# Optimization experiments

Hardware: AMD Instinct MI355X
Metric: run time of the kernel (lower is better)

The kernel has to match this reference:

```python
import jax, jax.numpy as jnp
import numpy as np

B, NQ, D = 8, 900, 256
NH, NL, NP = 8, 4, 4
DFF = 1024
DH = D // NH
SHAPES = [(100, 100), (50, 50), (25, 25), (13, 13)]
LV = sum(h * w for h, w in SHAPES)


def setup_inputs() -> dict:
    key = jax.random.key(0)
    ks = iter(jax.random.split(key, 40))
    nrm = lambda shape, s=0.02: jax.random.normal(next(ks), shape, jnp.float32) * s
    starts = np.cumsum([0] + [h * w for h, w in SHAPES[:-1]])
    return {
        'query': jax.random.normal(next(ks), (B, NQ, D), jnp.float32),
        'reference_points': jax.random.uniform(next(ks), (B, NQ, NL, 2), jnp.float32),
        'memory': jax.random.normal(next(ks), (B, LV, D), jnp.float32),
        'memory_spatial_shapes': jnp.array(SHAPES, jnp.int32),
        'level_start_index': jnp.array(starts, jnp.int32),
        'memory_key_padding_mask': jnp.zeros((B, LV), bool),
        'in_proj_w': nrm((3 * D, D)), 'in_proj_b': jnp.zeros((3 * D,), jnp.float32),
        'out_proj_w': nrm((D, D)), 'out_proj_b': jnp.zeros((D,), jnp.float32),
        'ln1_g': jnp.ones((D,), jnp.float32), 'ln1_b': jnp.zeros((D,), jnp.float32),
        'value_proj_w': nrm((D, D)), 'value_proj_b': jnp.zeros((D,), jnp.float32),
        'samp_off_w': nrm((NH * NL * NP * 2, D)), 'samp_off_b': nrm((NH * NL * NP * 2,), 1.0),
        'attn_w_w': nrm((NH * NL * NP, D)), 'attn_w_b': jnp.zeros((NH * NL * NP,), jnp.float32),
        'ca_out_w': nrm((D, D)), 'ca_out_b': jnp.zeros((D,), jnp.float32),
        'ln2_g': jnp.ones((D,), jnp.float32), 'ln2_b': jnp.zeros((D,), jnp.float32),
        'ffn_w1': nrm((DFF, D)), 'ffn_b1': jnp.zeros((DFF,), jnp.float32),
        'ffn_w2': nrm((D, DFF)), 'ffn_b2': jnp.zeros((D,), jnp.float32),
        'ln3_g': jnp.ones((D,), jnp.float32), 'ln3_b': jnp.zeros((D,), jnp.float32),
    }


def layer_norm(x, g, b):
    m = x.mean(-1, keepdims=True)
    v = jnp.var(x, axis=-1, keepdims=True)
    return (x - m) * jax.lax.rsqrt(v + 1e-5) * g + b


def self_attention(x, in_w, in_b, out_w, out_b):
    qkv = x @ in_w.T + in_b
    q, k, v = jnp.split(qkv, 3, axis=-1)
    b, n, _ = x.shape
    q = q.reshape(b, n, NH, DH)
    k = k.reshape(b, n, NH, DH)
    v = v.reshape(b, n, NH, DH)
    scores = jnp.einsum('bqhd,bkhd->bhqk', q, k) / jnp.sqrt(jnp.float32(DH))
    attn = jax.nn.softmax(scores, axis=-1)
    o = jnp.einsum('bhqk,bkhd->bqhd', attn, v).reshape(b, n, D)
    return o @ out_w.T + out_b


def ms_deform_attn(value, shapes, loc, aw):
    # value: (B, Lv, NH, DH); loc: (B, Nq, NH, NL, NP, 2) in [0,1]; aw: (B, Nq, NH, NL, NP)
    b, _, nh, dh = value.shape
    nq, p = loc.shape[1], loc.shape[4]
    acc = jnp.zeros((b, nh, nq, dh), value.dtype)
    start = 0
    for lvl, (hl, wl) in enumerate(shapes):
        v = value[:, start:start + hl * wl].transpose(0, 2, 1, 3)  # (B, NH, HW, DH)
        start += hl * wl
        g = loc[:, :, :, lvl]                      # (B, Nq, NH, NP, 2)
        x = g[..., 0] * wl - 0.5
        y = g[..., 1] * hl - 0.5
        x0 = jnp.floor(x); y0 = jnp.floor(y)
        lx = x - x0; ly = y - y0

        def gather(yi, xi):
            valid = (yi >= 0) & (yi < hl) & (xi >= 0) & (xi < wl)
            idx = (jnp.clip(yi, 0, hl - 1) * wl + jnp.clip(xi, 0, wl - 1)).astype(jnp.int32)
            idx = idx.transpose(0, 2, 1, 3).reshape(b, nh, nq * p)
            out = jnp.take_along_axis(v, idx[..., None], axis=2)  # (B, NH, Nq*NP, DH)
            m = valid.transpose(0, 2, 1, 3).reshape(b, nh, nq * p, 1)
            return jnp.where(m, out, 0.0)

        def w_(w):  # (B,Nq,NH,NP) -> (B,NH,Nq*NP,1)
            return w.transpose(0, 2, 1, 3).reshape(b, nh, nq * p, 1)

        samp = (gather(y0, x0) * w_((1 - lx) * (1 - ly))
                + gather(y0, x0 + 1) * w_(lx * (1 - ly))
                + gather(y0 + 1, x0) * w_((1 - lx) * ly)
                + gather(y0 + 1, x0 + 1) * w_(lx * ly))
        samp = samp.reshape(b, nh, nq, p, dh)
        wl_attn = aw[:, :, :, lvl].transpose(0, 2, 1, 3)  # (B, NH, Nq, NP)
        acc = acc + jnp.einsum('bhqpd,bhqp->bhqd', samp, wl_attn)
    return acc.transpose(0, 2, 1, 3).reshape(b, nq, nh * dh)


def reference(query, reference_points, memory, memory_spatial_shapes, level_start_index,
              memory_key_padding_mask, in_proj_w, in_proj_b, out_proj_w, out_proj_b,
              ln1_g, ln1_b, value_proj_w, value_proj_b, samp_off_w, samp_off_b,
              attn_w_w, attn_w_b, ca_out_w, ca_out_b, ln2_g, ln2_b,
              ffn_w1, ffn_b1, ffn_w2, ffn_b2, ln3_g, ln3_b):
    shapes = [(int(h), int(w)) for h, w in np.asarray(memory_spatial_shapes)]
    b, nq, _ = query.shape

    # self-attention + LN residual
    q_sa = self_attention(query, in_proj_w, in_proj_b, out_proj_w, out_proj_b)
    query = layer_norm(query + q_sa, ln1_g, ln1_b)

    # deformable cross-attention
    value = memory @ value_proj_w.T + value_proj_b
    value = jnp.where(memory_key_padding_mask[..., None], 0.0, value)
    value = value.reshape(b, -1, NH, DH)
    offsets = (query @ samp_off_w.T + samp_off_b).reshape(b, nq, NH, NL, NP, 2)
    aw = (query @ attn_w_w.T + attn_w_b).reshape(b, nq, NH, NL * NP)
    aw = jax.nn.softmax(aw, axis=-1).reshape(b, nq, NH, NL, NP)
    normalizer = jnp.stack([memory_spatial_shapes[:, 1], memory_spatial_shapes[:, 0]], -1).astype(query.dtype)  # (NL,2)=(W,H)
    loc = reference_points[:, :, None, :, None, :] + offsets / normalizer[None, None, None, :, None, :]
    q_ca = ms_deform_attn(value, shapes, loc, aw) @ ca_out_w.T + ca_out_b
    query = layer_norm(query + q_ca, ln2_g, ln2_b)

    # FFN + LN residual
    q_ffn = jax.nn.relu(query @ ffn_w1.T + ffn_b1) @ ffn_w2.T + ffn_b2
    return layer_norm(query + q_ffn, ln3_g, ln3_b)
```

## Files before the change

### kernel.cpp

```cpp
#include <hip/hip_runtime.h>
#include <cstddef>

namespace {

constexpr int kB   = 8;
constexpr int kNQ  = 900;
constexpr int kD   = 256;
constexpr int kDFF = 1024;
constexpr int kLV  = 13294;

typedef short bf16x8 __attribute__((ext_vector_type(8)));
typedef float f32x4  __attribute__((ext_vector_type(4)));

__device__ inline unsigned short f2bf(float f) {
  union { float f; unsigned u; } v; v.f = f;
  return (unsigned short)((v.u + 0x7FFF + ((v.u >> 16) & 1)) >> 16);
}

__device__ inline float bf2f(unsigned short u) {
  union { unsigned u; float f; } v; v.u = (unsigned)u << 16;
  return v.f;
}

__device__ inline unsigned cvt_pk_bf16(float a, float b) {
  unsigned r;
  asm("v_cvt_pk_bf16_f32 %0, %1, %2" : "=v"(r) : "v"(a), "v"(b));
  return r;
}

__global__ __launch_bounds__(256) void f32_to_bf16_kernel(
    const float* __restrict__ in, unsigned* __restrict__ out, int n8) {
  int i = blockIdx.x * 256 + threadIdx.x;
  const int stride = gridDim.x * 256;
  for (; i < n8; i += stride) {
    const float4 a = ((const float4*)in)[(size_t)i * 2];
    const float4 b = ((const float4*)in)[(size_t)i * 2 + 1];
    uint4 r;
    r.x = cvt_pk_bf16(a.x, a.y);
    r.y = cvt_pk_bf16(a.z, a.w);
    r.z = cvt_pk_bf16(b.x, b.y);
    r.w = cvt_pk_bf16(b.z, b.w);
    ((uint4*)out)[i] = r;
  }
}

__global__ __launch_bounds__(256, 2) void gemm_val2_kernel(
    const unsigned short* __restrict__ A, const float* __restrict__ W,
    const float* __restrict__ bias, unsigned short* __restrict__ C, int M) {
  __shared__ short Ws[128 * 256];

  const int t  = threadIdx.x;
  const int w  = t >> 6;
  const int l  = t & 63;
  const int lr = l & 15;
  const int lc = l >> 4;
  const int col  = (int)(blockIdx.x >> 8);
  const int slot = (int)(blockIdx.x & 255);
  const int bn = col * 128;
  const int wm = (w >> 1) * 64;
  const int wn = (w & 1) * 64;

#pragma unroll 4
  for (int i = 0; i < 16; ++i) {
    const int idx = i * 256 + t;
    const int row = idx >> 5;
    const int c16 = idx & 31;
    const float* wp = W + (size_t)(bn + row) * 256 + c16 * 8;
    const float4 w0 = *(const float4*)wp;
    const float4 w1 = *(const float4*)(wp + 4);
    uint4 p;
    p.x = cvt_pk_bf16(w0.x, w0.y);
    p.y = cvt_pk_bf16(w0.z, w0.w);
    p.z = cvt_pk_bf16(w1.x, w1.y);
    p.w = cvt_pk_bf16(w1.z, w1.w);
    const int boff = (row * 512 + c16 * 16) ^ ((row & 7) << 4);
    *(uint4*)((char*)Ws + boff) = p;
  }
  __syncthreads();

  float bv[4];
#pragma unroll
  for (int n = 0; n < 4; ++n) bv[n] = bias[bn + wn + n * 16 + lr];

  for (int tile = slot; tile * 128 < M; tile += 256) {
    const int bm = tile * 128;

    const unsigned short* apm[4];
#pragma unroll
    for (int m = 0; m < 4; ++m) {
      int row = bm + wm + m * 16 + lr;
      row = row < M ? row : M - 1;
      apm[m] = A + (size_t)row * 256 + lc * 8;
    }
    bf16x8 af[8][4];
#pragma unroll
    for (int kk = 0; kk < 8; ++kk)
#pragma unroll
      for (int m = 0; m < 4; ++m)
        af[kk][m] = *(const bf16x8*)(apm[m] + kk * 32);

    f32x4 acc[4][4];
#pragma unroll
    for (int m = 0; m < 4; ++m)
#pragma unroll
      for (int n = 0; n < 4; ++n) acc[m][n] = (f32x4){0.f, 0.f, 0.f, 0.f};

#pragma unroll
    for (int kk = 0; kk < 8; ++kk) {
      const int kb = kk * 64 + lc * 16;
      bf16x8 bfr[4];
#pragma unroll
      for (int n = 0; n < 4; ++n) {
        const int row = wn + n * 16 + lr;
        const int boff = (row * 512 + kb) ^ ((row & 7) << 4);
        bfr[n] = *(const bf16x8*)((const char*)Ws + boff);
      }
#pragma unroll
      for (int m = 0; m < 4; ++m)
#pragma unroll
        for (int n = 0; n < 4; ++n)
          acc[m][n] = __builtin_amdgcn_mfma_f32_16x16x32_bf16(af[kk][m], bfr[n], acc[m][n], 0, 0, 0);
    }

#pragma unroll
    for (int m = 0; m < 4; ++m) {
      const int rbase = bm + wm + m * 16 + lc * 4;
#pragma unroll
      for (int n = 0; n < 4; ++n) {
        const int cidx = bn + wn + n * 16 + lr;
#pragma unroll
        for (int j = 0; j < 4; ++j) {
          const int r = rbase + j;
          if (r < M) C[(size_t)r * 256 + cidx] = f2bf(acc[m][n][j] + bv[n]);
        }
      }
    }
  }
}

__global__ __launch_bounds__(256) void gemm_mfma_kernel(
    const float* __restrict__ A, const float* __restrict__ W,
    const float* __restrict__ bias, void* __restrict__ Cv,
    int M, int N, int K, int relu, int out_bf16) {
  __shared__ short As[128 * 64];
  __shared__ short Bs[128 * 64];

  const int t  = threadIdx.x;
  const int bm = blockIdx.y * 128;
  const int bn = blockIdx.x * 128;
  const int w  = t >> 6;
  const int l  = t & 63;
  const int wm = (w >> 1) * 64;
  const int wn = (w & 1) * 64;

  f32x4 acc[4][4];
#pragma unroll
  for (int m = 0; m < 4; ++m)
#pragma unroll
    for (int n = 0; n < 4; ++n) acc[m][n] = (f32x4){0.f, 0.f, 0.f, 0.f};

  float4 pa[8], pw[8];
  auto load_tile = [&](int k0) {
#pragma unroll
    for (int i = 0; i < 8; ++i) {
      const int slot = i * 256 + t;
      const int row  = slot >> 4;
      const int c4   = slot & 15;
      const int ar   = bm + row;
      pa[i] = (ar < M) ? *(const float4*)(A + (size_t)ar * K + k0 + c4 * 4)
                       : make_float4(0.f, 0.f, 0.f, 0.f);
      pw[i] = *(const float4*)(W + (size_t)(bn + row) * K + k0 + c4 * 4);
    }
  };

  load_tile(0);

  for (int k0 = 0;;) {
#pragma unroll
    for (int i = 0; i < 8; ++i) {
      const int slot = i * 256 + t;
      const int row  = slot >> 4;
      const int c4   = slot & 15;
      const int boff = (row * 128 + c4 * 8) ^ ((row & 7) << 4);
      uint2 ap;
      ap.x = cvt_pk_bf16(pa[i].x, pa[i].y);
      ap.y = cvt_pk_bf16(pa[i].z, pa[i].w);
      *(uint2*)((char*)As + boff) = ap;
      uint2 wp;
      wp.x = cvt_pk_bf16(pw[i].x, pw[i].y);
      wp.y = cvt_pk_bf16(pw[i].z, pw[i].w);
      *(uint2*)((char*)Bs + boff) = wp;
    }
    __syncthreads();

    const int knext = k0 + 64;
    if (knext < K) load_tile(knext);

#pragma unroll
    for (int ks = 0; ks < 2; ++ks) {
      const int koff = (ks * 32 + (l >> 4) * 8) * 2;
      bf16x8 af[4], bfr[4];
#pragma unroll
      for (int m = 0; m < 4; ++m) {
        const int row = wm + m * 16 + (l & 15);
        af[m] = *(const bf16x8*)((const char*)As + ((row * 128 + koff) ^ ((row & 7) << 4)));
      }
#pragma unroll
      for (int n = 0; n < 4; ++n) {
        const int row = wn + n * 16 + (l & 15);
        bfr[n] = *(const bf16x8*)((const char*)Bs + ((row * 128 + koff) ^ ((row & 7) << 4)));
      }
#pragma unroll
      for (int m = 0; m < 4; ++m)
#pragma unroll
        for (int n = 0; n < 4; ++n)
          acc[m][n] = __builtin_amdgcn_mfma_f32_16x16x32_bf16(af[m], bfr[n], acc[m][n], 0, 0, 0);
    }

    k0 = knext;
    if (k0 >= K) break;
    __syncthreads();
  }

  const int lr4 = (l >> 4) * 4;
  const int lc  = l & 15;
#pragma unroll
  for (int m = 0; m < 4; ++m) {
    const int rbase = bm + wm + m * 16 + lr4;
#pragma unroll
    for (int n = 0; n < 4; ++n) {
      const int col = bn + wn + n * 16 + lc;
      const float bv = bias[col];
#pragma unroll
      for (int j = 0; j < 4; ++j) {
        const int r = rbase + j;
        if (r < M) {
          float v = acc[m][n][j] + bv;
          if (relu) v = fmaxf(v, 0.f);
          if (out_bf16)
            ((unsigned short*)Cv)[(size_t)r * N + col] = f2bf(v);
          else
            ((float*)Cv)[(size_t)r * N + col] = v;
        }
      }
    }
  }
}

__global__ __launch_bounds__(256) void gemm_qoff_kernel(
    const float* __restrict__ A, const float* __restrict__ soW,
    const float* __restrict__ soB, const float* __restrict__ awW,
    const float* __restrict__ awB, float* __restrict__ offs,
    float* __restrict__ awr, int M) {
  __shared__ short As[128 * 64];
  __shared__ short Bs[128 * 64];

  const int t  = threadIdx.x;
  const int bm = blockIdx.y * 128;
  const int bn = blockIdx.x * 128;
  const int w  = t >> 6;
  const int l  = t & 63;
  const int wm = (w >> 1) * 64;
  const int wn = (w & 1) * 64;

  f32x4 acc[4][4];
#pragma unroll
  for (int m = 0; m < 4; ++m)
#pragma unroll
    for (int n = 0; n < 4; ++n) acc[m][n] = (f32x4){0.f, 0.f, 0.f, 0.f};

  float4 pa[8], pw[8];
  auto load_tile = [&](int k0) {
#pragma unroll
    for (int i = 0; i < 8; ++i) {
      const int slot = i * 256 + t;
      const int row  = slot >> 4;
      const int c4   = slot & 15;
      const int ar   = bm + row;
      pa[i] = (ar < M) ? *(const float4*)(A + (size_t)ar * 256 + k0 + c4 * 4)
                       : make_float4(0.f, 0.f, 0.f, 0.f);
      const int gn = bn + row;
      const float* Wp = (gn < 256) ? (soW + (size_t)gn * 256)
                                   : (awW + (size_t)(gn - 256) * 256);
      pw[i] = *(const float4*)(Wp + k0 + c4 * 4);
    }
  };

  load_tile(0);

  for (int k0 = 0;;) {
#pragma unroll
    for (int i = 0; i < 8; ++i) {
      const int slot = i * 256 + t;
      const int row  = slot >> 4;
      const int c4   = slot & 15;
      const int boff = (row * 128 + c4 * 8) ^ ((row & 7) << 4);
      uint2 ap;
      ap.x = cvt_pk_bf16(pa[i].x, pa[i].y);
      ap.y = cvt_pk_bf16(pa[i].z, pa[i].w);
      *(uint2*)((char*)As + boff) = ap;
      uint2 wp;
      wp.x = cvt_pk_bf16(pw[i].x, pw[i].y);
      wp.y = cvt_pk_bf16(pw[i].z, pw[i].w);
      *(uint2*)((char*)Bs + boff) = wp;
    }
    __syncthreads();

    const int knext = k0 + 64;
    if (knext < 256) load_tile(knext);

#pragma unroll
    for (int ks = 0; ks < 2; ++ks) {
      const int koff = (ks * 32 + (l >> 4) * 8) * 2;
      bf16x8 af[4], bfr[4];
#pragma unroll
      for (int m = 0; m < 4; ++m) {
        const int row = wm + m * 16 + (l & 15);
        af[m] = *(const bf16x8*)((const char*)As + ((row * 128 + koff) ^ ((row & 7) << 4)));
      }
#pragma unroll
      for (int n = 0; n < 4; ++n) {
        const int row = wn + n * 16 + (l & 15);
        bfr[n] = *(const bf16x8*)((const char*)Bs + ((row * 128 + koff) ^ ((row & 7) << 4)));
      }
#pragma unroll
      for (int m = 0; m < 4; ++m)
#pragma unroll
        for (int n = 0; n < 4; ++n)
          acc[m][n] = __builtin_amdgcn_mfma_f32_16x16x32_bf16(af[m], bfr[n], acc[m][n], 0, 0, 0);
    }

    k0 = knext;
    if (k0 >= 256) break;
    __syncthreads();
  }

  const int lr4 = (l >> 4) * 4;
  const int lc  = l & 15;
#pragma unroll
  for (int m = 0; m < 4; ++m) {
    const int rbase = bm + wm + m * 16 + lr4;
#pragma unroll
    for (int n = 0; n < 4; ++n) {
      const int col = bn + wn + n * 16 + lc;
      const float bv = (col < 256) ? soB[col] : awB[col - 256];
#pragma unroll
      for (int j = 0; j < 4; ++j) {
        const int r = rbase + j;
        if (r < M) {
          const float v = acc[m][n][j] + bv;
          if (col < 256) offs[(size_t)r * 256 + col] = v;
          else           awr[(size_t)r * 128 + col - 256] = v;
        }
      }
    }
  }
}

__global__ __launch_bounds__(256) void self_attn_mfma_kernel(
    const unsigned short* __restrict__ qkv, float* __restrict__ out) {
  const int b = blockIdx.y >> 3;
  const int h = blockIdx.y & 7;
  const int t = threadIdx.x;
  const int w = t >> 6;
  const int l = t & 63;
  const int lr = l & 15;
  const int lc = l >> 4;

  __shared__ short Klds[64 * 40];
  __shared__ short Vt[32 * 68];
  __shared__ short Plds[4][2 * 16 * 68];

  const float scale = 0.17677669529663687f;
  const int qb0 = blockIdx.x * 128 + w * 16;

  bf16x8 qf[2] = {};
#pragma unroll
  for (int qt = 0; qt < 2; ++qt) {
    const int qr = qb0 + qt * 64 + lr;
    if (qr < kNQ)
      qf[qt] = *(const bf16x8*)(qkv + ((size_t)(b * kNQ + qr)) * 768 + h * 32 + lc * 8);
  }

  f32x4 o[2][2];
#pragma unroll
  for (int qt = 0; qt < 2; ++qt)
#pragma unroll
    for (int dh = 0; dh < 2; ++dh) o[qt][dh] = (f32x4){0.f, 0.f, 0.f, 0.f};
  const f32x4 zero4 = {0.f, 0.f, 0.f, 0.f};
  float lsum[2] = {0.f, 0.f};

  const int skey = t & 63, sc = t >> 6;
  bf16x8 kreg = {}, vreg = {};
  auto load_kv = [&](int tb) {
    const int kr = tb + skey;
    if (kr < kNQ) {
      const unsigned short* p = qkv + ((size_t)(b * kNQ + kr)) * 768 + h * 32 + sc * 8;
      kreg = *(const bf16x8*)(p + 256);
      vreg = *(const bf16x8*)(p + 512);
    } else {
      kreg = (bf16x8){}; vreg = (bf16x8){};
    }
  };

  load_kv(0);

  for (int tb = 0; tb < kNQ; tb += 64) {
    *(bf16x8*)&Klds[skey * 40 + sc * 8] = kreg;
#pragma unroll
    for (int i = 0; i < 8; ++i) Vt[(sc * 8 + i) * 68 + skey] = vreg[i];
    __syncthreads();

    if (tb + 64 < kNQ) load_kv(tb + 64);

    f32x4 s[2][4];
#pragma unroll
    for (int kt = 0; kt < 4; ++kt) {
      bf16x8 kf = *(const bf16x8*)&Klds[(kt * 16 + lr) * 40 + lc * 8];
      s[0][kt] = __builtin_amdgcn_mfma_f32_16x16x32_bf16(kf, qf[0], zero4, 0, 0, 0);
      s[1][kt] = __builtin_amdgcn_mfma_f32_16x16x32_bf16(kf, qf[1], zero4, 0, 0, 0);
    }

#pragma unroll
    for (int qt = 0; qt < 2; ++qt) {
      short* Pw = Plds[w] + qt * (16 * 68);
      float ls = 0.f;
#pragma unroll
      for (int kt = 0; kt < 4; ++kt) {
        float p[4];
#pragma unroll
        for (int j = 0; j < 4; ++j) {
          const int kg = tb + kt * 16 + lc * 4 + j;
          const float e = __expf(s[qt][kt][j] * scale);
          p[j] = (kg < kNQ) ? e : 0.f;
          ls += p[j];
        }
        uint2 pk;
        pk.x = cvt_pk_bf16(p[0], p[1]);
        pk.y = cvt_pk_bf16(p[2], p[3]);
        *(uint2*)&Pw[lr * 68 + kt * 16 + lc * 4] = pk;
      }
      lsum[qt] += ls;
    }

    bf16x8 v00 = *(const bf16x8*)&Vt[lr * 68 + lc * 8];
    bf16x8 v01 = *(const bf16x8*)&Vt[lr * 68 + 32 + lc * 8];
    bf16x8 v10 = *(const bf16x8*)&Vt[(16 + lr) * 68 + lc * 8];
    bf16x8 v11 = *(const bf16x8*)&Vt[(16 + lr) * 68 + 32 + lc * 8];
#pragma unroll
    for (int qt = 0; qt < 2; ++qt) {
      const short* Pw = Plds[w] + qt * (16 * 68);
      bf16x8 pa0 = *(const bf16x8*)&Pw[lr * 68 + lc * 8];
      bf16x8 pa1 = *(const bf16x8*)&Pw[lr * 68 + 32 + lc * 8];
      o[qt][0] = __builtin_amdgcn_mfma_f32_16x16x32_bf16(pa0, v00, o[qt][0], 0, 0, 0);
      o[qt][0] = __builtin_amdgcn_mfma_f32_16x16x32_bf16(pa1, v01, o[qt][0], 0, 0, 0);
      o[qt][1] = __builtin_amdgcn_mfma_f32_16x16x32_bf16(pa0, v10, o[qt][1], 0, 0, 0);
      o[qt][1] = __builtin_amdgcn_mfma_f32_16x16x32_bf16(pa1, v11, o[qt][1], 0, 0, 0);
    }
    __syncthreads();
  }

#pragma unroll
  for (int qt = 0; qt < 2; ++qt) {
    float lt = lsum[qt];
    lt += __shfl_xor(lt, 16);
    lt += __shfl_xor(lt, 32);
#pragma unroll
    for (int j = 0; j < 4; ++j) {
      const float lq = __shfl(lt, lc * 4 + j);
      const int q = qb0 + qt * 64 + lc * 4 + j;
      if (q < kNQ) {
        const float inv = 1.f / lq;
        float* op = out + ((size_t)(b * kNQ + q)) * 256 + h * 32;
        op[lr]      = o[qt][0][j] * inv;
        op[16 + lr] = o[qt][1][j] * inv;
      }
    }
  }
}

__global__ __launch_bounds__(256) void ln_res_kernel(
    const float* __restrict__ x, const float* __restrict__ res,
    const float* __restrict__ g, const float* __restrict__ bta,
    float* __restrict__ out) {
  const int row = blockIdx.x;
  const int t = threadIdx.x;
  const size_t idx = (size_t)row * 256 + t;
  const float v = x[idx] + res[idx];
  float s = v, s2 = v * v;
#pragma unroll
  for (int mask = 1; mask < 64; mask <<= 1) {
    s  += __shfl_xor(s, mask);
    s2 += __shfl_xor(s2, mask);
  }
  __shared__ float ws[4], ws2[4];
  if ((t & 63) == 0) { ws[t >> 6] = s; ws2[t >> 6] = s2; }
  __syncthreads();
  const float S  = ws[0] + ws[1] + ws[2] + ws[3];
  const float S2 = ws2[0] + ws2[1] + ws2[2] + ws2[3];
  const float mean = S * (1.f / 256.f);
  const float var  = S2 * (1.f / 256.f) - mean * mean;
  const float rstd = rsqrtf(var + 1e-5f);
  out[idx] = (v - mean) * rstd * g[t] + bta[t];
}

__global__ __launch_bounds__(256) void deform_kernel(
    const unsigned short* __restrict__ value,
    const float* __restrict__ offs,
    const float* __restrict__ awr,
    const float* __restrict__ refp,
    float* __restrict__ out) {
  const int bq = blockIdx.x;
  const int b = bq / kNQ;
  const int t = threadIdx.x;

  __shared__ int2  cpk[128][4];
  __shared__ float part[4][256];

  if (t < 128) {
    const float a = awr[(size_t)bq * 128 + t];
    float mx = a;
#pragma unroll
    for (int mask = 1; mask < 16; mask <<= 1) mx = fmaxf(mx, __shfl_xor(mx, mask));
    const float e = __expf(a - mx);
    float se = e;
#pragma unroll
    for (int mask = 1; mask < 16; mask <<= 1) se += __shfl_xor(se, mask);
    const float aw = e / se;

    const int h = t >> 4, lp = t & 15, lvl = lp >> 2;
    const int HL[4] = {100, 50, 25, 13};
    const int WL[4] = {100, 50, 25, 13};
    const int ST[4] = {0, 10000, 12500, 13125};
    const int Hl = HL[lvl], Wl = WL[lvl], st = ST[lvl];
    const float rx = refp[((size_t)bq * 4 + lvl) * 2 + 0];
    const float ry = refp[((size_t)bq * 4 + lvl) * 2 + 1];
    const float ox = offs[(size_t)bq * 256 + h * 32 + lp * 2 + 0];
    const float oy = offs[(size_t)bq * 256 + h * 32 + lp * 2 + 1];
    const float x = rx * (float)Wl + ox - 0.5f;
    const float y = ry * (float)Hl + oy - 0.5f;
    const float x0f = floorf(x), y0f = floorf(y);
    const int x0 = (int)x0f, y0 = (int)y0f;
    const float lx = x - x0f, ly = y - y0f;
    const float wts[4] = {(1.f - lx) * (1.f - ly), lx * (1.f - ly),
                          (1.f - lx) * ly,         lx * ly};
    const int ys[4] = {y0, y0, y0 + 1, y0 + 1};
    const int xs[4] = {x0, x0 + 1, x0, x0 + 1};
    const int pos = lp * 8 + h;
#pragma unroll
    for (int c = 0; c < 4; ++c) {
      const int yy = ys[c], xx = xs[c];
      const bool valid = (yy >= 0) && (yy < Hl) && (xx >= 0) && (xx < Wl);
      const int yc = min(max(yy, 0), Hl - 1);
      const int xc = min(max(xx, 0), Wl - 1);
      const float wf = valid ? wts[c] * aw : 0.f;
      cpk[pos][c] = make_int2(st + yc * Wl + xc, __float_as_int(wf));
    }
  }
  __syncthreads();

  const int w  = t >> 6;
  const int q4 = t & 63;
  const int h  = q4 >> 3;
  const int ch = q4 * 4;
  const unsigned short* vb = value + (size_t)b * kLV * 256 + ch;

  float a0 = 0.f, a1 = 0.f, a2 = 0.f, a3 = 0.f;
#pragma unroll
  for (int si = 0; si < 4; ++si) {
    const int s = w * 4 + si;
#pragma unroll
    for (int c = 0; c < 4; ++c) {
      const int2 p = cpk[s * 8 + h][c];
      const float wt = __int_as_float(p.y);
      const uint2 v = *(const uint2*)(vb + (size_t)p.x * 256);
      a0 = fmaf(wt, bf2f((unsigned short)(v.x & 0xffff)), a0);
      a1 = fmaf(wt, bf2f((unsigned short)(v.x >> 16)), a1);
      a2 = fmaf(wt, bf2f((unsigned short)(v.y & 0xffff)), a2);
      a3 = fmaf(wt, bf2f((unsigned short)(v.y >> 16)), a3);
    }
  }
  *(float4*)&part[w][ch] = make_float4(a0, a1, a2, a3);
  __syncthreads();

  out[(size_t)bq * 256 + t] = part[0][t] + part[1][t] + part[2][t] + part[3][t];
}

}

extern "C" void kernel_launch(void* const* d_in, const int* in_sizes, int n_in,
                              void* d_out, int out_size, void* d_ws, size_t ws_size,
                              hipStream_t stream) {
  const float* query  = (const float*)d_in[0];
  const float* refp   = (const float*)d_in[1];
  const float* memory = (const float*)d_in[2];
  const float* in_w  = (const float*)d_in[6];
  const float* in_b  = (const float*)d_in[7];
  const float* out_w = (const float*)d_in[8];
  const float* out_b = (const float*)d_in[9];
  const float* ln1g  = (const float*)d_in[10];
  const float* ln1b  = (const float*)d_in[11];
  const float* vp_w  = (const float*)d_in[12];
  const float* vp_b  = (const float*)d_in[13];
  const float* so_w  = (const float*)d_in[14];
  const float* so_b  = (const float*)d_in[15];
  const float* aw_w  = (const float*)d_in[16];
  const float* aw_b  = (const float*)d_in[17];
  const float* ca_w  = (const float*)d_in[18];
  const float* ca_b  = (const float*)d_in[19];
  const float* ln2g  = (const float*)d_in[20];
  const float* ln2b  = (const float*)d_in[21];
  const float* f1_w  = (const float*)d_in[22];
  const float* f1_b  = (const float*)d_in[23];
  const float* f2_w  = (const float*)d_in[24];
  const float* f2_b  = (const float*)d_in[25];
  const float* ln3g  = (const float*)d_in[26];
  const float* ln3b  = (const float*)d_in[27];
  float* out = (float*)d_out;

  const int MQ = kB * kNQ;
  const int MV = kB * kLV;

  float* ws = (float*)d_ws;
  size_t o = 0;
  float* qkvr = ws;
  float* ffh  = ws;  o += (size_t)MQ * kDFF;
  float* sa   = ws + o;  o += (size_t)MQ * kD;
  float* q1   = ws + o;  o += (size_t)MQ * kD;
  float* valr = ws + o;  o += (size_t)MV * kD;
  float* offs = ws + o;  o += (size_t)MQ * kD;
  float* awr  = ws + o;  o += (size_t)MQ * 128;
  float* dfo  = ws + o;  o += (size_t)MQ * kD;
  float* q2   = ws + o;  o += (size_t)MQ * kD;
  float* tmp  = ws + o;  o += (size_t)MQ * kD;
  (void)ws_size; (void)in_sizes; (void)n_in; (void)out_size;

  unsigned short* qkv_bf = (unsigned short*)qkvr;
  unsigned short* val_bf = (unsigned short*)valr;
  unsigned short* m_bf   = (unsigned short*)(valr + (size_t)MV * kD / 2);

  const dim3 blk(256);
  auto g128 = [](int M, int N) { return dim3((unsigned)((N + 127) / 128), (unsigned)((M + 127) / 128)); };

  f32_to_bf16_kernel<<<2048, blk, 0, stream>>>(memory, (unsigned*)m_bf, MV * kD / 8);
  gemm_mfma_kernel<<<g128(MQ, 768), blk, 0, stream>>>(query, in_w, in_b, qkv_bf, MQ, 768, kD, 0, 1);
  self_attn_mfma_kernel<<<dim3((kNQ + 127) / 128, kB * 8), blk, 0, stream>>>(qkv_bf, sa);
  gemm_mfma_kernel<<<g128(MQ, kD), blk, 0, stream>>>(sa, out_w, out_b, tmp, MQ, kD, kD, 0, 0);
  ln_res_kernel<<<MQ, blk, 0, stream>>>(query, tmp, ln1g, ln1b, q1);
  gemm_val2_kernel<<<512, blk, 0, stream>>>(m_bf, vp_w, vp_b, val_bf, MV);
  gemm_qoff_kernel<<<dim3(3, (MQ + 127) / 128), blk, 0, stream>>>(
      q1, so_w, so_b, aw_w, aw_b, offs, awr, MQ);
  deform_kernel<<<MQ, blk, 0, stream>>>(val_bf, offs, awr, refp, dfo);
  gemm_mfma_kernel<<<g128(MQ, kD), blk, 0, stream>>>(dfo, ca_w, ca_b, tmp, MQ, kD, kD, 0, 0);
  ln_res_kernel<<<MQ, blk, 0, stream>>>(q1, tmp, ln2g, ln2b, q2);
  gemm_mfma_kernel<<<g128(MQ, kDFF), blk, 0, stream>>>(q2, f1_w, f1_b, ffh, MQ, kDFF, kD, 1, 0);
  gemm_mfma_kernel<<<g128(MQ, kD), blk, 0, stream>>>(ffh, f2_w, f2_b, tmp, MQ, kD, kDFF, 0, 0);
  ln_res_kernel<<<MQ, blk, 0, stream>>>(q2, tmp, ln3g, ln3b, out);
}
```

Measured before the change: 288.3 us.

## Fuse output GEMMs with residual LayerNorm and store FFN hidden in bf16

Adds a gemm_ln_kernel that computes a full 256-wide output row tile (16 rows per block) and applies bias, residual add and LayerNorm in the epilogue. It replaces the three GEMM+ln_res_kernel pairs, removing the tmp buffer round trip and three launches. The FFN hidden activation is now written as bf16 and read directly, halving that traffic. The trade-off is that each 16-row block reconverts the whole fp32 weight tile to bf16, which adds redundant weight loads and conversion work, and the small M tile lowers MFMA reuse.

```diff
diff --git a/kernel.cpp b/kernel.cpp
--- a/kernel.cpp
+++ b/kernel.cpp
@@ -247,6 +247,124 @@
   }
 }
 
+__global__ __launch_bounds__(256) void gemm_ln_kernel(
+    const void* __restrict__ Av, const float* __restrict__ W,
+    const float* __restrict__ bias, const float* __restrict__ res,
+    const float* __restrict__ g, const float* __restrict__ beta,
+    float* __restrict__ C, int M, int K, int a_bf16) {
+  __shared__ short As[16 * 64];
+  __shared__ short Bs[256 * 64];
+  __shared__ float pS[4][16], pS2[4][16];
+
+  const int t  = threadIdx.x;
+  const int w  = t >> 6;
+  const int l  = t & 63;
+  const int lr = l & 15;
+  const int lc = l >> 4;
+  const int bm = blockIdx.x * 16;
+  const int wn = w * 64;
+
+  f32x4 acc[4];
+#pragma unroll
+  for (int n = 0; n < 4; ++n) acc[n] = (f32x4){0.f, 0.f, 0.f, 0.f};
+
+  for (int k0 = 0; k0 < K; k0 += 64) {
+    if (a_bf16) {
+      if (t < 128) {
+        const int row = t >> 3, c8 = t & 7;
+        const bf16x8 av = *(const bf16x8*)((const unsigned short*)Av +
+                                           (size_t)(bm + row) * K + k0 + c8 * 8);
+        const int boff = (row * 128 + c8 * 16) ^ ((row & 7) << 4);
+        *(bf16x8*)((char*)As + boff) = av;
+      }
+    } else {
+      const int row = t >> 4, c4 = t & 15;
+      const float4 av = *(const float4*)((const float*)Av +
+                                         (size_t)(bm + row) * K + k0 + c4 * 4);
+      uint2 p;
+      p.x = cvt_pk_bf16(av.x, av.y);
+      p.y = cvt_pk_bf16(av.z, av.w);
+      const int boff = (row * 128 + c4 * 8) ^ ((row & 7) << 4);
+      *(uint2*)((char*)As + boff) = p;
+    }
+#pragma unroll
+    for (int i = 0; i < 16; ++i) {
+      const int slot = i * 256 + t;
+      const int row = slot >> 4, c4 = slot & 15;
+      const float4 wv = *(const float4*)(W + (size_t)row * K + k0 + c4 * 4);
+      uint2 p;
+      p.x = cvt_pk_bf16(wv.x, wv.y);
+      p.y = cvt_pk_bf16(wv.z, wv.w);
+      const int boff = (row * 128 + c4 * 8) ^ ((row & 7) << 4);
+      *(uint2*)((char*)Bs + boff) = p;
+    }
+    __syncthreads();
+
+#pragma unroll
+    for (int ks = 0; ks < 2; ++ks) {
+      const int koff = (ks * 32 + lc * 8) * 2;
+      const bf16x8 af = *(const bf16x8*)((const char*)As + ((lr * 128 + koff) ^ ((lr & 7) << 4)));
+      bf16x8 bfr[4];
+#pragma unroll
+      for (int n = 0; n < 4; ++n) {
+        const int row = wn + n * 16 + lr;
+        bfr[n] = *(const bf16x8*)((const char*)Bs + ((row * 128 + koff) ^ ((row & 7) << 4)));
+      }
+#pragma unroll
+      for (int n = 0; n < 4; ++n)
+        acc[n] = __builtin_amdgcn_mfma_f32_16x16x32_bf16(af, bfr[n], acc[n], 0, 0, 0);
+    }
+    __syncthreads();
+  }
+
+  float bv[4], gl[4], bl[4];
+#pragma unroll
+  for (int n = 0; n < 4; ++n) {
+    const int col = wn + n * 16 + lr;
+    bv[n] = bias[col];
+    gl[n] = g[col];
+    bl[n] = beta[col];
+  }
+
+  float v[4][4];
+#pragma unroll
+  for (int j = 0; j < 4; ++j) {
+    const int grow = bm + lc * 4 + j;
+    float sj = 0.f, s2j = 0.f;
+#pragma unroll
+    for (int n = 0; n < 4; ++n) {
+      const int col = wn + n * 16 + lr;
+      const float vv = acc[n][j] + bv[n] + res[(size_t)grow * 256 + col];
+      v[j][n] = vv;
+      sj += vv;
+      s2j += vv * vv;
+    }
+#pragma unroll
+    for (int mask = 1; mask < 16; mask <<= 1) {
+      sj  += __shfl_xor(sj, mask);
+      s2j += __shfl_xor(s2j, mask);
+    }
+    if (lr == 0) { pS[w][lc * 4 + j] = sj; pS2[w][lc * 4 + j] = s2j; }
+  }
+  __syncthreads();
+
+#pragma unroll
+  for (int j = 0; j < 4; ++j) {
+    const int r16 = lc * 4 + j;
+    const float S  = pS[0][r16] + pS[1][r16] + pS[2][r16] + pS[3][r16];
+    const float S2 = pS2[0][r16] + pS2[1][r16] + pS2[2][r16] + pS2[3][r16];
+    const float mean = S * (1.f / 256.f);
+    const float var  = S2 * (1.f / 256.f) - mean * mean;
+    const float rstd = rsqrtf(var + 1e-5f);
+    const int grow = bm + lc * 4 + j;
+#pragma unroll
+    for (int n = 0; n < 4; ++n) {
+      const int col = wn + n * 16 + lr;
+      C[(size_t)grow * 256 + col] = (v[j][n] - mean) * rstd * gl[n] + bl[n];
+    }
+  }
+}
+
 __global__ __launch_bounds__(256) void gemm_qoff_kernel(
     const float* __restrict__ A, const float* __restrict__ soW,
     const float* __restrict__ soB, const float* __restrict__ awW,
@@ -477,31 +595,6 @@
       }
     }
   }
-}
-
-__global__ __launch_bounds__(256) void ln_res_kernel(
-    const float* __restrict__ x, const float* __restrict__ res,
-    const float* __restrict__ g, const float* __restrict__ bta,
-    float* __restrict__ out) {
-  const int row = blockIdx.x;
-  const int t = threadIdx.x;
-  const size_t idx = (size_t)row * 256 + t;
-  const float v = x[idx] + res[idx];
-  float s = v, s2 = v * v;
-#pragma unroll
-  for (int mask = 1; mask < 64; mask <<= 1) {
-    s  += __shfl_xor(s, mask);
-    s2 += __shfl_xor(s2, mask);
-  }
-  __shared__ float ws[4], ws2[4];
-  if ((t & 63) == 0) { ws[t >> 6] = s; ws2[t >> 6] = s2; }
-  __syncthreads();
-  const float S  = ws[0] + ws[1] + ws[2] + ws[3];
-  const float S2 = ws2[0] + ws2[1] + ws2[2] + ws2[3];
-  const float mean = S * (1.f / 256.f);
-  const float var  = S2 * (1.f / 256.f) - mean * mean;
-  const float rstd = rsqrtf(var + 1e-5f);
-  out[idx] = (v - mean) * rstd * g[t] + bta[t];
 }
 
 __global__ __launch_bounds__(256) void deform_kernel(
@@ -624,7 +717,7 @@
   float* ws = (float*)d_ws;
   size_t o = 0;
   float* qkvr = ws;
-  float* ffh  = ws;  o += (size_t)MQ * kDFF;
+  o += (size_t)MQ * kDFF;
   float* sa   = ws + o;  o += (size_t)MQ * kD;
   float* q1   = ws + o;  o += (size_t)MQ * kD;
   float* valr = ws + o;  o += (size_t)MV * kD;
@@ -632,10 +725,10 @@
   float* awr  = ws + o;  o += (size_t)MQ * 128;
   float* dfo  = ws + o;  o += (size_t)MQ * kD;
   float* q2   = ws + o;  o += (size_t)MQ * kD;
-  float* tmp  = ws + o;  o += (size_t)MQ * kD;
   (void)ws_size; (void)in_sizes; (void)n_in; (void)out_size;
 
   unsigned short* qkv_bf = (unsigned short*)qkvr;
+  unsigned short* ffh_bf = (unsigned short*)qkvr;
   unsigned short* val_bf = (unsigned short*)valr;
   unsigned short* m_bf   = (unsigned short*)(valr + (size_t)MV * kD / 2);
 
@@ -645,15 +738,12 @@
   f32_to_bf16_kernel<<<2048, blk, 0, stream>>>(memory, (unsigned*)m_bf, MV * kD / 8);
   gemm_mfma_kernel<<<g128(MQ, 768), blk, 0, stream>>>(query, in_w, in_b, qkv_bf, MQ, 768, kD, 0, 1);
   self_attn_mfma_kernel<<<dim3((kNQ + 127) / 128, kB * 8), blk, 0, stream>>>(qkv_bf, sa);
-  gemm_mfma_kernel<<<g128(MQ, kD), blk, 0, stream>>>(sa, out_w, out_b, tmp, MQ, kD, kD, 0, 0);
-  ln_res_kernel<<<MQ, blk, 0, stream>>>(query, tmp, ln1g, ln1b, q1);
+  gemm_ln_kernel<<<MQ / 16, blk, 0, stream>>>(sa, out_w, out_b, query, ln1g, ln1b, q1, MQ, kD, 0);
   gemm_val2_kernel<<<512, blk, 0, stream>>>(m_bf, vp_w, vp_b, val_bf, MV);
   gemm_qoff_kernel<<<dim3(3, (MQ + 127) / 128), blk, 0, stream>>>(
       q1, so_w, so_b, aw_w, aw_b, offs, awr, MQ);
   deform_kernel<<<MQ, blk, 0, stream>>>(val_bf, offs, awr, refp, dfo);
-  gemm_mfma_kernel<<<g128(MQ, kD), blk, 0, stream>>>(dfo, ca_w, ca_b, tmp, MQ, kD, kD, 0, 0);
-  ln_res_kernel<<<MQ, blk, 0, stream>>>(q1, tmp, ln2g, ln2b, q2);
-  gemm_mfma_kernel<<<g128(MQ, kDFF), blk, 0, stream>>>(q2, f1_w, f1_b, ffh, MQ, kDFF, kD, 1, 0);
-  gemm_mfma_kernel<<<g128(MQ, kD), blk, 0, stream>>>(ffh, f2_w, f2_b, tmp, MQ, kD, kDFF, 0, 0);
-  ln_res_kernel<<<MQ, blk, 0, stream>>>(q2, tmp, ln3g, ln3b, out);
-}
+  gemm_ln_kernel<<<MQ / 16, blk, 0, stream>>>(dfo, ca_w, ca_b, q1, ln2g, ln2b, q2, MQ, kD, 0);
+  gemm_mfma_kernel<<<g128(MQ, kDFF), blk, 0, stream>>>(q2, f1_w, f1_b, ffh_bf, MQ, kDFF, kD, 1, 1);
+  gemm_ln_kernel<<<MQ / 16, blk, 0, stream>>>(ffh_bf, f2_w, f2_b, q2, ln3g, ln3b, out, MQ, kDFF, 1);
+}
```

Result: slower. 384.7 us (+33.5%).
